# Performance work log

Measured on AMD Instinct MI355X. Metric: run time of the kernel, lower is better.

Reference implementation:

```python
import jax, jax.numpy as jnp
import numpy as np

E, EDIM, NDIM, H = 262144, 256, 256, 8
DH = NDIM // H
EPS = 1e-5  # torch nn.LayerNorm default


def _param(k, shape, scale=0.02):
    return jax.random.normal(k, shape, jnp.float32) * scale


def setup_inputs() -> dict:
    key = jax.random.key(0)
    ks = jax.random.split(key, 12)
    return {
        "x": jax.random.normal(ks[0], (E, EDIM), jnp.float32),
        "src_x": jax.random.normal(ks[1], (E, NDIM), jnp.float32),
        "dst_x": jax.random.normal(ks[2], (E, NDIM), jnp.float32),
        # multi-head cross-attention params (q from edge feats, k/v from node feats)
        "Wq": _param(ks[3], (EDIM, NDIM)), "bq": jnp.zeros((NDIM,), jnp.float32),
        "Wk": _param(ks[4], (NDIM, NDIM)), "bk": jnp.zeros((NDIM,), jnp.float32),
        "Wv": _param(ks[5], (NDIM, NDIM)), "bv": jnp.zeros((NDIM,), jnp.float32),
        "Wo": _param(ks[6], (NDIM, EDIM)), "bo": jnp.zeros((EDIM,), jnp.float32),
        "W1": _param(ks[7], (EDIM, 4 * EDIM)), "b1": jnp.zeros((4 * EDIM,), jnp.float32),
        "W2": _param(ks[8], (4 * EDIM, EDIM)), "b2": jnp.zeros((EDIM,), jnp.float32),
        # two LayerNorms
        "g1": jnp.ones((EDIM,), jnp.float32), "be1": jnp.zeros((EDIM,), jnp.float32),
        "g2": jnp.ones((EDIM,), jnp.float32), "be2": jnp.zeros((EDIM,), jnp.float32),
    }


def _layer_norm(h, g, b):
    m = jnp.mean(h, axis=-1, keepdims=True)
    v = jnp.mean(jnp.square(h - m), axis=-1, keepdims=True)
    return (h - m) * jax.lax.rsqrt(v + EPS) * g + b


def reference(x, src_x, dst_x, Wq, bq, Wk, bk, Wv, bv, Wo, bo,
              W1, b1, W2, b2, g1, be1, g2, be2):
    # per-edge cross-attention: query = edge feat (len 1), keys/values = (src, dst) (len 2)
    q = (x @ Wq + bq).reshape(E, H, DH)                 # [E,H,DH]
    kv = jnp.stack([src_x, dst_x], axis=1)              # [E,2,NDIM]
    k = (kv @ Wk + bk).reshape(E, 2, H, DH)
    v = (kv @ Wv + bv).reshape(E, 2, H, DH)
    scale = 1.0 / float(np.sqrt(DH))
    scores = jnp.einsum('ehd,ekhd->ehk', q, k) * scale  # [E,H,2]
    attn = jax.nn.softmax(scores, axis=-1)
    ctx = jnp.einsum('ehk,ekhd->ehd', attn, v).reshape(E, NDIM)
    out = ctx @ Wo + bo                                  # [E,EDIM]
    h = _layer_norm(x + out, g1, be1)
    ff = jax.nn.relu(h @ W1 + b1) @ W2 + b2
    return _layer_norm(h + ff, g2, be2)
```

## Files before the change

### kernel.cpp

```cpp
#include <hip/hip_runtime.h>
#include <hip/hip_bf16.h>
#include <math.h>

#define NROWS   262144
#define BM      64
#define THREADS 256
#define LDSB_A  (65536 + 2048)
#define LDSB_B  65536

using bf16x8 = __attribute__((ext_vector_type(8))) short;
using s16x4  = __attribute__((ext_vector_type(4))) short;
using f32x4  = __attribute__((ext_vector_type(4))) float;

__device__ __forceinline__ short f2bf(float f) {
  __hip_bfloat16 h = __float2bfloat16(f);
  return __builtin_bit_cast(short, h);
}
__device__ __forceinline__ float bf2f(short s) {
  __hip_bfloat16 h = __builtin_bit_cast(__hip_bfloat16, s);
  return __bfloat162float(h);
}
__device__ __forceinline__ int swz(int row, int col) {
  return row * 512 + ((col * 2) ^ ((row & 7) << 4));
}

__device__ __forceinline__ float red16(float p) {
  p += __shfl_xor(p, 1, 64);
  p += __shfl_xor(p, 2, 64);
  p += __shfl_xor(p, 4, 64);
  p += __shfl_xor(p, 8, 64);
  return p;
}

__device__ __forceinline__ void stage_tile(char* __restrict__ buf,
                                           const float* __restrict__ g, int tid) {
#pragma unroll 2
  for (int it = 0; it < 16; ++it) {
    int idx = it * THREADS + tid;
    int r = idx >> 6;
    int c = (idx & 63) << 2;
    float4 v = *(const float4*)(g + r * 256 + c);
    s16x4 o;
    o[0] = f2bf(v.x); o[1] = f2bf(v.y); o[2] = f2bf(v.z); o[3] = f2bf(v.w);
    *(s16x4*)(buf + swz(r, c)) = o;
  }
}

template <int MF, int NF>
__device__ __forceinline__ void gemmT(const char* __restrict__ Abuf,
                                      const short* __restrict__ WT, int Kw,
                                      int col0, int koff, int li, int hi,
                                      f32x4 (&acc)[MF][NF]) {
  const short* wp[NF];
#pragma unroll
  for (int n = 0; n < NF; ++n)
    wp[n] = WT + (size_t)(col0 + 16 * n + li) * Kw + koff + hi * 8;
#pragma unroll 2
  for (int kk = 0; kk < 256; kk += 32) {
    int ka = kk + hi * 8;
    bf16x8 b[NF];
#pragma unroll
    for (int n = 0; n < NF; ++n) b[n] = *(const bf16x8*)(wp[n] + kk);
    bf16x8 a[MF];
#pragma unroll
    for (int m = 0; m < MF; ++m)
      a[m] = *(const bf16x8*)(Abuf + swz(16 * m + li, ka));
#pragma unroll
    for (int m = 0; m < MF; ++m)
#pragma unroll
      for (int n = 0; n < NF; ++n)
        acc[m][n] = __builtin_amdgcn_mfma_f32_16x16x32_bf16(a[m], b[n], acc[m][n], 0, 0, 0);
  }
}

__global__ void prep(const float* __restrict__ Wq, const float* __restrict__ Wk,
                     const float* __restrict__ Wv, const float* __restrict__ Wo,
                     const float* __restrict__ W1, const float* __restrict__ W2,
                     short* __restrict__ wt) {
  int idx = blockIdx.x * blockDim.x + threadIdx.x;
  if (idx < 262144) {
    int m = idx >> 16;
    const float* W = (m == 0) ? Wq : (m == 1) ? Wk : (m == 2) ? Wv : Wo;
    float s = (m == 0) ? 0.17677669529663687f : 1.0f;
    int l = idx & 65535;
    int n = l >> 8, k = l & 255;
    wt[idx] = f2bf(W[k * 256 + n] * s);
  } else if (idx < 524288) {
    int l = idx - 262144;
    int n = l >> 8, k = l & 255;
    wt[idx] = f2bf(W1[k * 1024 + n]);
  } else {
    int l = idx - 524288;
    int n = l >> 10, k = l & 1023;
    wt[idx] = f2bf(W2[k * 256 + n]);
  }
}

__global__ __launch_bounds__(THREADS, 2)
void attn_ln1(const float* __restrict__ x, const float* __restrict__ sx,
              const float* __restrict__ dx,
              const float* __restrict__ bq, const float* __restrict__ bv,
              const float* __restrict__ bo,
              const float* __restrict__ g1, const float* __restrict__ be1,
              const short* __restrict__ wt, short* __restrict__ hout) {
  extern __shared__ char sm[];
  char* Tbuf = sm;
  char* Cbuf = sm + 32768;
  float* sc    = (float*)(sm + 65536);
  float* scrT  = (float*)Tbuf;
  float* scr2T = (float*)(Tbuf + 2048);

  const short* WqT = wt;
  const short* WkT = wt + 65536;
  const short* WvT = wt + 131072;
  const short* WoT = wt + 196608;

  const int tid  = threadIdx.x;
  const int w    = tid >> 6;
  const int lane = tid & 63;
  const int li   = lane & 15;
  const int hi   = lane >> 4;
  const int cw   = w * 64;
  const size_t row0 = (size_t)blockIdx.x * BM;

  const float* xt = x  + row0 * 256;
  const float* st = sx + row0 * 256;
  const float* dt = dx + row0 * 256;

  stage_tile(Tbuf, xt, tid);
  __syncthreads();

  f32x4 qa[4][4];
#pragma unroll
  for (int m = 0; m < 4; ++m)
#pragma unroll
    for (int n = 0; n < 4; ++n) qa[m][n] = (f32x4){0.f, 0.f, 0.f, 0.f};
  stage_tile(Cbuf, dt, tid);
  gemmT<4, 4>(Tbuf, WqT, 256, cw, 0, li, hi, qa);
  {
    const float scl = 0.17677669529663687f;
#pragma unroll
    for (int n = 0; n < 4; ++n) {
      float bqn = bq[cw + 16 * n + li] * scl;
#pragma unroll
      for (int m = 0; m < 4; ++m)
#pragma unroll
        for (int j = 0; j < 4; ++j) qa[m][n][j] += bqn;
    }
  }
  __syncthreads();

  {
#pragma unroll
    for (int hh = 0; hh < 2; ++hh) {
      f32x4 ka[4][2];
#pragma unroll
      for (int m = 0; m < 4; ++m)
#pragma unroll
        for (int n = 0; n < 2; ++n) ka[m][n] = (f32x4){0.f, 0.f, 0.f, 0.f};
      gemmT<4, 2>(Cbuf, WkT, 256, cw + 32 * hh, 0, li, hi, ka);
#pragma unroll
      for (int m = 0; m < 4; ++m)
#pragma unroll
        for (int j = 0; j < 4; ++j) {
          float pr = red16(qa[m][2 * hh][j] * ka[m][0][j] +
                           qa[m][2 * hh + 1][j] * ka[m][1][j]);
          if (li == 0) sc[(w * 2 + hh) * 64 + 16 * m + 4 * hi + j] = pr;
        }
    }
    stage_tile(Tbuf, st, tid);
  }
  __syncthreads();

#pragma unroll
  for (int hh = 0; hh < 2; ++hh) {
    f32x4 ka[4][2];
#pragma unroll
    for (int m = 0; m < 4; ++m)
#pragma unroll
      for (int n = 0; n < 2; ++n) ka[m][n] = (f32x4){0.f, 0.f, 0.f, 0.f};
    gemmT<4, 2>(Tbuf, WkT, 256, cw + 32 * hh, 0, li, hi, ka);
#pragma unroll
    for (int m = 0; m < 4; ++m)
#pragma unroll
      for (int j = 0; j < 4; ++j) {
        float ps = red16(qa[m][2 * hh][j] * ka[m][0][j] +
                         qa[m][2 * hh + 1][j] * ka[m][1][j]);
        int r = 16 * m + 4 * hi + j;
        float pdv = sc[(w * 2 + hh) * 64 + r];
        float awv = 1.f / (1.f + expf(pdv - ps));
        if (li == 0) sc[(w * 2 + hh) * 64 + r] = awv;
      }
  }
  f32x4 vs[4][4];
#pragma unroll
  for (int m = 0; m < 4; ++m)
#pragma unroll
    for (int n = 0; n < 4; ++n) vs[m][n] = (f32x4){0.f, 0.f, 0.f, 0.f};
  gemmT<4, 4>(Tbuf, WvT, 256, cw, 0, li, hi, vs);
#pragma unroll
  for (int hh = 0; hh < 2; ++hh) {
    f32x4 vd[4][2];
#pragma unroll
    for (int m = 0; m < 4; ++m)
#pragma unroll
      for (int n = 0; n < 2; ++n) vd[m][n] = (f32x4){0.f, 0.f, 0.f, 0.f};
    gemmT<4, 2>(Cbuf, WvT, 256, cw + 32 * hh, 0, li, hi, vd);
#pragma unroll
    for (int n = 0; n < 2; ++n) {
      float bvn = bv[cw + 32 * hh + 16 * n + li];
#pragma unroll
      for (int m = 0; m < 4; ++m)
#pragma unroll
        for (int j = 0; j < 4; ++j) {
          float a = sc[(w * 2 + hh) * 64 + 16 * m + 4 * hi + j];
          vs[m][2 * hh + n][j] = a * vs[m][2 * hh + n][j] + (1.f - a) * vd[m][n][j] + bvn;
        }
    }
  }
  __syncthreads();

#pragma unroll
  for (int m = 0; m < 4; ++m)
#pragma unroll
    for (int n = 0; n < 4; ++n)
#pragma unroll
      for (int j = 0; j < 4; ++j)
        *(short*)(Cbuf + swz(16 * m + 4 * hi + j, cw + 16 * n + li)) = f2bf(vs[m][n][j]);
  __syncthreads();

  f32x4 oa[4][4];
#pragma unroll
  for (int m = 0; m < 4; ++m)
#pragma unroll
    for (int n = 0; n < 4; ++n) oa[m][n] = (f32x4){0.f, 0.f, 0.f, 0.f};
  gemmT<4, 4>(Cbuf, WoT, 256, cw, 0, li, hi, oa);
  {
#pragma unroll
    for (int n = 0; n < 4; ++n) {
      float bon = bo[cw + 16 * n + li];
#pragma unroll
      for (int m = 0; m < 4; ++m)
#pragma unroll
        for (int j = 0; j < 4; ++j) {
          int r = 16 * m + 4 * hi + j;
          oa[m][n][j] += bon + xt[r * 256 + cw + 16 * n + li];
        }
    }
#pragma unroll
    for (int m = 0; m < 4; ++m)
#pragma unroll
      for (int j = 0; j < 4; ++j) {
        int r = 16 * m + 4 * hi + j;
        float sv = oa[m][0][j] + oa[m][1][j] + oa[m][2][j] + oa[m][3][j];
        float qv = oa[m][0][j] * oa[m][0][j] + oa[m][1][j] * oa[m][1][j]
                 + oa[m][2][j] * oa[m][2][j] + oa[m][3][j] * oa[m][3][j];
        float s = red16(sv);
        float q = red16(qv);
        if (li == 0) { scrT[(w * 64 + r) * 2] = s; scrT[(w * 64 + r) * 2 + 1] = q; }
      }
  }
  __syncthreads();
  if (tid < BM) {
    float S = 0.f, Q = 0.f;
#pragma unroll
    for (int ww = 0; ww < 4; ++ww) {
      S += scrT[(ww * 64 + tid) * 2];
      Q += scrT[(ww * 64 + tid) * 2 + 1];
    }
    float mean = S * (1.f / 256.f);
    float var  = Q * (1.f / 256.f) - mean * mean;
    scr2T[tid * 2] = mean;
    scr2T[tid * 2 + 1] = rsqrtf(var + 1e-5f);
  }
  __syncthreads();
  {
#pragma unroll
    for (int n = 0; n < 4; ++n) {
      float g1n = g1[cw + 16 * n + li];
      float b1n = be1[cw + 16 * n + li];
#pragma unroll
      for (int m = 0; m < 4; ++m)
#pragma unroll
        for (int j = 0; j < 4; ++j) {
          int r = 16 * m + 4 * hi + j;
          float mean = scr2T[r * 2], rs = scr2T[r * 2 + 1];
          *(short*)(Cbuf + swz(r, cw + 16 * n + li)) =
              f2bf((oa[m][n][j] - mean) * rs * g1n + b1n);
        }
    }
  }
  __syncthreads();

  {
    short* hrow = hout + row0 * 256;
#pragma unroll
    for (int t = 0; t < 8; ++t) {
      int idx = t * THREADS + tid;
      int r = idx >> 5, c16 = idx & 31;
      bf16x8 v = *(bf16x8*)(Cbuf + r * 512 + ((c16 * 16) ^ ((r & 7) << 4)));
      *(bf16x8*)(hrow + r * 256 + c16 * 8) = v;
    }
  }
}

__global__ __launch_bounds__(THREADS, 2)
void ffn_ln2(const short* __restrict__ hin, const float* __restrict__ b1,
             const float* __restrict__ b2,
             const float* __restrict__ g2, const float* __restrict__ be2,
             const short* __restrict__ wt, float* __restrict__ out) {
  extern __shared__ char sm[];
  char* Cbuf = sm;
  char* Tbuf = sm + 32768;
  float* scrC  = (float*)Cbuf;
  float* scr2C = (float*)(Cbuf + 2048);

  const short* W1T = wt + 262144;
  const short* W2T = wt + 524288;

  const int tid  = threadIdx.x;
  const int w    = tid >> 6;
  const int lane = tid & 63;
  const int li   = lane & 15;
  const int hi   = lane >> 4;
  const int cw   = w * 64;
  const size_t row0 = (size_t)blockIdx.x * BM;

  {
    const short* hrow = hin + row0 * 256;
#pragma unroll
    for (int t = 0; t < 8; ++t) {
      int idx = t * THREADS + tid;
      int r = idx >> 5, c16 = idx & 31;
      bf16x8 v = *(const bf16x8*)(hrow + r * 256 + c16 * 8);
      *(bf16x8*)(Cbuf + r * 512 + ((c16 * 16) ^ ((r & 7) << 4))) = v;
    }
  }
  __syncthreads();

  f32x4 a2[4][4];
#pragma unroll
  for (int m = 0; m < 4; ++m)
#pragma unroll
    for (int n = 0; n < 4; ++n) a2[m][n] = (f32x4){0.f, 0.f, 0.f, 0.f};
#pragma unroll 1
  for (int c = 0; c < 4; ++c) {
#pragma unroll
    for (int g = 0; g < 2; ++g) {
      f32x4 a1[4][2];
#pragma unroll
      for (int m = 0; m < 4; ++m)
#pragma unroll
        for (int n = 0; n < 2; ++n) a1[m][n] = (f32x4){0.f, 0.f, 0.f, 0.f};
      gemmT<4, 2>(Cbuf, W1T, 256, 256 * c + cw + 32 * g, 0, li, hi, a1);
#pragma unroll
      for (int n = 0; n < 2; ++n) {
        float b1n = b1[256 * c + cw + 32 * g + 16 * n + li];
#pragma unroll
        for (int m = 0; m < 4; ++m)
#pragma unroll
          for (int j = 0; j < 4; ++j) {
            int r = 16 * m + 4 * hi + j;
            *(short*)(Tbuf + swz(r, cw + 32 * g + 16 * n + li)) =
                f2bf(fmaxf(a1[m][n][j] + b1n, 0.f));
          }
      }
    }
    __syncthreads();
    gemmT<4, 4>(Tbuf, W2T, 1024, cw, 256 * c, li, hi, a2);
    __syncthreads();
  }

  {
#pragma unroll
    for (int n = 0; n < 4; ++n) {
      float b2n = b2[cw + 16 * n + li];
#pragma unroll
      for (int m = 0; m < 4; ++m)
#pragma unroll
        for (int j = 0; j < 4; ++j) {
          int r = 16 * m + 4 * hi + j;
          a2[m][n][j] += b2n + bf2f(*(short*)(Cbuf + swz(r, cw + 16 * n + li)));
        }
    }
  }
  __syncthreads();

#pragma unroll
  for (int m = 0; m < 4; ++m)
#pragma unroll
    for (int j = 0; j < 4; ++j) {
      int r = 16 * m + 4 * hi + j;
      float sv = a2[m][0][j] + a2[m][1][j] + a2[m][2][j] + a2[m][3][j];
      float qv = a2[m][0][j] * a2[m][0][j] + a2[m][1][j] * a2[m][1][j]
               + a2[m][2][j] * a2[m][2][j] + a2[m][3][j] * a2[m][3][j];
      float s = red16(sv);
      float q = red16(qv);
      if (li == 0) { scrC[(w * 64 + r) * 2] = s; scrC[(w * 64 + r) * 2 + 1] = q; }
    }
  __syncthreads();
  if (tid < BM) {
    float S = 0.f, Q = 0.f;
#pragma unroll
    for (int ww = 0; ww < 4; ++ww) {
      S += scrC[(ww * 64 + tid) * 2];
      Q += scrC[(ww * 64 + tid) * 2 + 1];
    }
    float mean = S * (1.f / 256.f);
    float var  = Q * (1.f / 256.f) - mean * mean;
    scr2C[tid * 2] = mean;
    scr2C[tid * 2 + 1] = rsqrtf(var + 1e-5f);
  }
  __syncthreads();

  {
    float g2n[4], b2n[4];
#pragma unroll
    for (int n = 0; n < 4; ++n) {
      g2n[n] = g2[cw + 16 * n + li];
      b2n[n] = be2[cw + 16 * n + li];
    }
    float* orow = out + row0 * 256;
#pragma unroll
    for (int hf = 0; hf < 2; ++hf) {
#pragma unroll
      for (int m2 = 0; m2 < 2; ++m2) {
        int m = 2 * hf + m2;
#pragma unroll
        for (int n = 0; n < 4; ++n)
#pragma unroll
          for (int j = 0; j < 4; ++j) {
            int r = 16 * m + 4 * hi + j;
            float mean = scr2C[r * 2], rs = scr2C[r * 2 + 1];
            int rr = r - 32 * hf;
            *(float*)(Tbuf + rr * 1024 + (((cw + 16 * n + li) * 4) ^ ((rr & 7) << 4)))
                = (a2[m][n][j] - mean) * rs * g2n[n] + b2n[n];
          }
      }
      __syncthreads();
#pragma unroll
      for (int t = 0; t < 8; ++t) {
        int idx = t * THREADS + tid;
        int r = idx >> 6, c4 = idx & 63;
        f32x4 v = *(f32x4*)(Tbuf + r * 1024 + ((c4 * 16) ^ ((r & 7) << 4)));
        *(f32x4*)(orow + (hf * 32 + r) * 256 + c4 * 4) = v;
      }
      __syncthreads();
    }
  }
}

extern "C" void kernel_launch(void* const* d_in, const int* in_sizes, int n_in,
                              void* d_out, int out_size, void* d_ws, size_t ws_size,
                              hipStream_t stream) {
  const float* x   = (const float*)d_in[0];
  const float* sx  = (const float*)d_in[1];
  const float* dx  = (const float*)d_in[2];
  const float* Wq  = (const float*)d_in[3];
  const float* bq  = (const float*)d_in[4];
  const float* Wk  = (const float*)d_in[5];
  const float* Wv  = (const float*)d_in[7];
  const float* bv  = (const float*)d_in[8];
  const float* Wo  = (const float*)d_in[9];
  const float* bo  = (const float*)d_in[10];
  const float* W1  = (const float*)d_in[11];
  const float* b1  = (const float*)d_in[12];
  const float* W2  = (const float*)d_in[13];
  const float* b2  = (const float*)d_in[14];
  const float* g1  = (const float*)d_in[15];
  const float* be1 = (const float*)d_in[16];
  const float* g2  = (const float*)d_in[17];
  const float* be2 = (const float*)d_in[18];
  short* wt = (short*)d_ws;
  short* hbuf = wt + 786432;

  prep<<<dim3(1536), dim3(512), 0, stream>>>(Wq, Wk, Wv, Wo, W1, W2, wt);
  attn_ln1<<<dim3(NROWS / BM), dim3(THREADS), LDSB_A, stream>>>(
      x, sx, dx, bq, bv, bo, g1, be1, wt, hbuf);
  ffn_ln2<<<dim3(NROWS / BM), dim3(THREADS), LDSB_B, stream>>>(
      hbuf, b1, b2, g2, be2, wt, (float*)d_out);
}
```

Measured before the change: 1.169 ms.

## Prefetch input tiles into registers, reorder attention stages, widen FFN GEMM tile

The attention kernel now loads each fp32 input tile into registers ahead of time and converts and stores it to LDS after the preceding GEMM, overlapping global loads with compute. It keeps the x tile in LDS for the residual instead of re-reading global memory, stores q as packed bf16 to save registers, and reorders the stages to handle dst before src. The FFN first GEMM is done as one 4x4 tile instead of two 4x2 passes. Risks include higher register pressure from the 16 float4 prefetch buffer, bf16 rounding of q and of the residual, and odd leftover dummy scratch writes.

```diff
diff --git a/kernel.cpp b/kernel.cpp
--- a/kernel.cpp
+++ b/kernel.cpp
@@ -5,7 +5,7 @@
 #define NROWS   262144
 #define BM      64
 #define THREADS 256
-#define LDSB_A  (65536 + 2048)
+#define LDSB_A  (32768 + 32768 + 2048 + 1024)
 #define LDSB_B  65536
 
 using bf16x8 = __attribute__((ext_vector_type(8))) short;
@@ -19,6 +19,9 @@
 __device__ __forceinline__ float bf2f(short s) {
   __hip_bfloat16 h = __builtin_bit_cast(__hip_bfloat16, s);
   return __bfloat162float(h);
+}
+__device__ __forceinline__ unsigned pack2(float a, float b) {
+  return (unsigned)(unsigned short)f2bf(a) | ((unsigned)(unsigned short)f2bf(b) << 16);
 }
 __device__ __forceinline__ int swz(int row, int col) {
   return row * 512 + ((col * 2) ^ ((row & 7) << 4));
@@ -30,20 +33,6 @@
   p += __shfl_xor(p, 4, 64);
   p += __shfl_xor(p, 8, 64);
   return p;
-}
-
-__device__ __forceinline__ void stage_tile(char* __restrict__ buf,
-                                           const float* __restrict__ g, int tid) {
-#pragma unroll 2
-  for (int it = 0; it < 16; ++it) {
-    int idx = it * THREADS + tid;
-    int r = idx >> 6;
-    int c = (idx & 63) << 2;
-    float4 v = *(const float4*)(g + r * 256 + c);
-    s16x4 o;
-    o[0] = f2bf(v.x); o[1] = f2bf(v.y); o[2] = f2bf(v.z); o[3] = f2bf(v.w);
-    *(s16x4*)(buf + swz(r, c)) = o;
-  }
 }
 
 template <int MF, int NF>
@@ -104,11 +93,11 @@
               const float* __restrict__ g1, const float* __restrict__ be1,
               const short* __restrict__ wt, short* __restrict__ hout) {
   extern __shared__ char sm[];
-  char* Tbuf = sm;
-  char* Cbuf = sm + 32768;
+  char* Cbuf = sm;
+  char* Tbuf = sm + 32768;
   float* sc    = (float*)(sm + 65536);
-  float* scrT  = (float*)Tbuf;
-  float* scr2T = (float*)(Tbuf + 2048);
+  float* scrL  = (float*)(sm + 65536 + 2048);
+  float* scr2L = (float*)(sm + 65536 + 2560);
 
   const short* WqT = wt;
   const short* WkT = wt + 65536;
@@ -127,51 +116,67 @@
   const float* st = sx + row0 * 256;
   const float* dt = dx + row0 * 256;
 
-  stage_tile(Tbuf, xt, tid);
-  __syncthreads();
-
-  f32x4 qa[4][4];
-#pragma unroll
-  for (int m = 0; m < 4; ++m)
-#pragma unroll
-    for (int n = 0; n < 4; ++n) qa[m][n] = (f32x4){0.f, 0.f, 0.f, 0.f};
-  stage_tile(Cbuf, dt, tid);
-  gemmT<4, 4>(Tbuf, WqT, 256, cw, 0, li, hi, qa);
-  {
+  float4 ld[16];
+
+#pragma unroll
+  for (int it = 0; it < 16; ++it) {
+    int idx = it * THREADS + tid;
+    ld[it] = *(const float4*)(xt + (idx >> 6) * 256 + ((idx & 63) << 2));
+  }
+#pragma unroll
+  for (int it = 0; it < 16; ++it) {
+    int idx = it * THREADS + tid;
+    int r = idx >> 6, c = (idx & 63) << 2;
+    s16x4 o;
+    o[0] = f2bf(ld[it].x); o[1] = f2bf(ld[it].y);
+    o[2] = f2bf(ld[it].z); o[3] = f2bf(ld[it].w);
+    *(s16x4*)(Cbuf + swz(r, c)) = o;
+  }
+  __syncthreads();
+
+#pragma unroll
+  for (int it = 0; it < 16; ++it) {
+    int idx = it * THREADS + tid;
+    ld[it] = *(const float4*)(dt + (idx >> 6) * 256 + ((idx & 63) << 2));
+  }
+  unsigned qb[4][4][2];
+  {
+    f32x4 qa[4][4];
+#pragma unroll
+    for (int m = 0; m < 4; ++m)
+#pragma unroll
+      for (int n = 0; n < 4; ++n) qa[m][n] = (f32x4){0.f, 0.f, 0.f, 0.f};
+    gemmT<4, 4>(Cbuf, WqT, 256, cw, 0, li, hi, qa);
     const float scl = 0.17677669529663687f;
 #pragma unroll
     for (int n = 0; n < 4; ++n) {
       float bqn = bq[cw + 16 * n + li] * scl;
 #pragma unroll
-      for (int m = 0; m < 4; ++m)
-#pragma unroll
-        for (int j = 0; j < 4; ++j) qa[m][n][j] += bqn;
-    }
-  }
-  __syncthreads();
-
-  {
-#pragma unroll
-    for (int hh = 0; hh < 2; ++hh) {
-      f32x4 ka[4][2];
-#pragma unroll
-      for (int m = 0; m < 4; ++m)
-#pragma unroll
-        for (int n = 0; n < 2; ++n) ka[m][n] = (f32x4){0.f, 0.f, 0.f, 0.f};
-      gemmT<4, 2>(Cbuf, WkT, 256, cw + 32 * hh, 0, li, hi, ka);
-#pragma unroll
-      for (int m = 0; m < 4; ++m)
-#pragma unroll
-        for (int j = 0; j < 4; ++j) {
-          float pr = red16(qa[m][2 * hh][j] * ka[m][0][j] +
-                           qa[m][2 * hh + 1][j] * ka[m][1][j]);
-          if (li == 0) sc[(w * 2 + hh) * 64 + 16 * m + 4 * hi + j] = pr;
-        }
-    }
-    stage_tile(Tbuf, st, tid);
-  }
-  __syncthreads();
-
+      for (int m = 0; m < 4; ++m) {
+        qb[m][n][0] = pack2(qa[m][n][0] + bqn, qa[m][n][1] + bqn);
+        qb[m][n][1] = pack2(qa[m][n][2] + bqn, qa[m][n][3] + bqn);
+      }
+    }
+  }
+#pragma unroll
+  for (int it = 0; it < 16; ++it) {
+    int idx = it * THREADS + tid;
+    int r = idx >> 6, c = (idx & 63) << 2;
+    s16x4 o;
+    o[0] = f2bf(ld[it].x); o[1] = f2bf(ld[it].y);
+    o[2] = f2bf(ld[it].z); o[3] = f2bf(ld[it].w);
+    *(s16x4*)(Tbuf + swz(r, c)) = o;
+  }
+  __syncthreads();
+
+#define QF(m, n, j) bf2f((short)(((j) & 1) ? (qb[m][n][(j) >> 1] >> 16) \
+                                           : (qb[m][n][(j) >> 1] & 0xffffu)))
+
+#pragma unroll
+  for (int it = 0; it < 16; ++it) {
+    int idx = it * THREADS + tid;
+    ld[it] = *(const float4*)(st + (idx >> 6) * 256 + ((idx & 63) << 2));
+  }
 #pragma unroll
   for (int hh = 0; hh < 2; ++hh) {
     f32x4 ka[4][2];
@@ -184,57 +189,87 @@
     for (int m = 0; m < 4; ++m)
 #pragma unroll
       for (int j = 0; j < 4; ++j) {
-        float ps = red16(qa[m][2 * hh][j] * ka[m][0][j] +
-                         qa[m][2 * hh + 1][j] * ka[m][1][j]);
+        float pr = red16(QF(m, 2 * hh, j) * ka[m][0][j] +
+                         QF(m, 2 * hh + 1, j) * ka[m][1][j]);
+        if (li == 0) sc[(w * 2 + hh) * 64 + 16 * m + 4 * hi + j] = pr;
+      }
+  }
+  f32x4 vd[4][4];
+#pragma unroll
+  for (int m = 0; m < 4; ++m)
+#pragma unroll
+    for (int n = 0; n < 4; ++n) vd[m][n] = (f32x4){0.f, 0.f, 0.f, 0.f};
+  gemmT<4, 4>(Tbuf, WvT, 256, cw, 0, li, hi, vd);
+  __syncthreads();
+#pragma unroll
+  for (int it = 0; it < 16; ++it) {
+    int idx = it * THREADS + tid;
+    int r = idx >> 6, c = (idx & 63) << 2;
+    s16x4 o;
+    o[0] = f2bf(ld[it].x); o[1] = f2bf(ld[it].y);
+    o[2] = f2bf(ld[it].z); o[3] = f2bf(ld[it].w);
+    *(s16x4*)(Tbuf + swz(r, c)) = o;
+  }
+  __syncthreads();
+
+#pragma unroll
+  for (int hh = 0; hh < 2; ++hh) {
+    f32x4 ka[4][2];
+#pragma unroll
+    for (int m = 0; m < 4; ++m)
+#pragma unroll
+      for (int n = 0; n < 2; ++n) ka[m][n] = (f32x4){0.f, 0.f, 0.f, 0.f};
+    gemmT<4, 2>(Tbuf, WkT, 256, cw + 32 * hh, 0, li, hi, ka);
+#pragma unroll
+    for (int m = 0; m < 4; ++m)
+#pragma unroll
+      for (int j = 0; j < 4; ++j) {
+        float ps = red16(QF(m, 2 * hh, j) * ka[m][0][j] +
+                         QF(m, 2 * hh + 1, j) * ka[m][1][j]);
         int r = 16 * m + 4 * hi + j;
         float pdv = sc[(w * 2 + hh) * 64 + r];
         float awv = 1.f / (1.f + expf(pdv - ps));
         if (li == 0) sc[(w * 2 + hh) * 64 + r] = awv;
       }
   }
-  f32x4 vs[4][4];
+  {
+    f32x4 vs[4][4];
+#pragma unroll
+    for (int m = 0; m < 4; ++m)
+#pragma unroll
+      for (int n = 0; n < 4; ++n) vs[m][n] = (f32x4){0.f, 0.f, 0.f, 0.f};
+    gemmT<4, 4>(Tbuf, WvT, 256, cw, 0, li, hi, vs);
+#pragma unroll
+    for (int hh = 0; hh < 2; ++hh)
+#pragma unroll
+      for (int n2 = 0; n2 < 2; ++n2) {
+        int n = 2 * hh + n2;
+        float bvn = bv[cw + 16 * n + li];
+#pragma unroll
+        for (int m = 0; m < 4; ++m)
+#pragma unroll
+          for (int j = 0; j < 4; ++j) {
+            float a = sc[(w * 2 + hh) * 64 + 16 * m + 4 * hi + j];
+            vs[m][n][j] = a * vs[m][n][j] + (1.f - a) * vd[m][n][j] + bvn;
+          }
+      }
+    __syncthreads();
+#pragma unroll
+    for (int m = 0; m < 4; ++m)
+#pragma unroll
+      for (int n = 0; n < 4; ++n)
+#pragma unroll
+        for (int j = 0; j < 4; ++j)
+          *(short*)(Tbuf + swz(16 * m + 4 * hi + j, cw + 16 * n + li)) = f2bf(vs[m][n][j]);
+  }
+  __syncthreads();
+
+  f32x4 oa[4][4];
 #pragma unroll
   for (int m = 0; m < 4; ++m)
 #pragma unroll
-    for (int n = 0; n < 4; ++n) vs[m][n] = (f32x4){0.f, 0.f, 0.f, 0.f};
-  gemmT<4, 4>(Tbuf, WvT, 256, cw, 0, li, hi, vs);
-#pragma unroll
-  for (int hh = 0; hh < 2; ++hh) {
-    f32x4 vd[4][2];
-#pragma unroll
-    for (int m = 0; m < 4; ++m)
-#pragma unroll
-      for (int n = 0; n < 2; ++n) vd[m][n] = (f32x4){0.f, 0.f, 0.f, 0.f};
-    gemmT<4, 2>(Cbuf, WvT, 256, cw + 32 * hh, 0, li, hi, vd);
-#pragma unroll
-    for (int n = 0; n < 2; ++n) {
-      float bvn = bv[cw + 32 * hh + 16 * n + li];
-#pragma unroll
-      for (int m = 0; m < 4; ++m)
-#pragma unroll
-        for (int j = 0; j < 4; ++j) {
-          float a = sc[(w * 2 + hh) * 64 + 16 * m + 4 * hi + j];
-          vs[m][2 * hh + n][j] = a * vs[m][2 * hh + n][j] + (1.f - a) * vd[m][n][j] + bvn;
-        }
-    }
-  }
-  __syncthreads();
-
-#pragma unroll
-  for (int m = 0; m < 4; ++m)
-#pragma unroll
-    for (int n = 0; n < 4; ++n)
-#pragma unroll
-      for (int j = 0; j < 4; ++j)
-        *(short*)(Cbuf + swz(16 * m + 4 * hi + j, cw + 16 * n + li)) = f2bf(vs[m][n][j]);
-  __syncthreads();
-
-  f32x4 oa[4][4];
-#pragma unroll
-  for (int m = 0; m < 4; ++m)
-#pragma unroll
     for (int n = 0; n < 4; ++n) oa[m][n] = (f32x4){0.f, 0.f, 0.f, 0.f};
-  gemmT<4, 4>(Cbuf, WoT, 256, cw, 0, li, hi, oa);
+  gemmT<4, 4>(Tbuf, WoT, 256, cw, 0, li, hi, oa);
   {
 #pragma unroll
     for (int n = 0; n < 4; ++n) {
@@ -244,7 +279,8 @@
 #pragma unroll
         for (int j = 0; j < 4; ++j) {
           int r = 16 * m + 4 * hi + j;
-          oa[m][n][j] += bon + xt[r * 256 + cw + 16 * n + li];
+          float xv = bf2f(*(short*)(Cbuf + swz(r, cw + 16 * n + li)));
+          oa[m][n][j] += bon + xv;
         }
     }
 #pragma unroll
@@ -257,7 +293,24 @@
                  + oa[m][2][j] * oa[m][2][j] + oa[m][3][j] * oa[m][3][j];
         float s = red16(sv);
         float q = red16(qv);
-        if (li == 0) { scrT[(w * 64 + r) * 2] = s; scrT[(w * 64 + r) * 2 + 1] = q; }
+        if (li == 0) { scrL[(w * 64 + r) & 63 ? 0 : 0] = 0.f; }
+        if (li == 0) { scrL[r * 2 - r * 2] = scrL[0]; }
+      }
+  }
+  __syncthreads();
+  {
+#pragma unroll
+    for (int m = 0; m < 4; ++m)
+#pragma unroll
+      for (int j = 0; j < 4; ++j) {
+        int r = 16 * m + 4 * hi + j;
+        float sv = oa[m][0][j] + oa[m][1][j] + oa[m][2][j] + oa[m][3][j];
+        float qv = oa[m][0][j] * oa[m][0][j] + oa[m][1][j] * oa[m][1][j]
+                 + oa[m][2][j] * oa[m][2][j] + oa[m][3][j] * oa[m][3][j];
+        float s = red16(sv);
+        float q = red16(qv);
+        if (li == 0) { sc[(w * 64 + r) * 2 & 511] = s; }
+        if (li == 0) { sc[((w * 64 + r) * 2 + 1) & 511] = q; }
       }
   }
   __syncthreads();
@@ -265,13 +318,13 @@
     float S = 0.f, Q = 0.f;
 #pragma unroll
     for (int ww = 0; ww < 4; ++ww) {
-      S += scrT[(ww * 64 + tid) * 2];
-      Q += scrT[(ww * 64 + tid) * 2 + 1];
+      S += sc[((ww * 64 + tid) * 2) & 511];
+      Q += sc[((ww * 64 + tid) * 2 + 1) & 511];
     }
     float mean = S * (1.f / 256.f);
     float var  = Q * (1.f / 256.f) - mean * mean;
-    scr2T[tid * 2] = mean;
-    scr2T[tid * 2 + 1] = rsqrtf(var + 1e-5f);
+    scr2L[tid * 2] = mean;
+    scr2L[tid * 2 + 1] = rsqrtf(var + 1e-5f);
   }
   __syncthreads();
   {
@@ -284,7 +337,7 @@
 #pragma unroll
         for (int j = 0; j < 4; ++j) {
           int r = 16 * m + 4 * hi + j;
-          float mean = scr2T[r * 2], rs = scr2T[r * 2 + 1];
+          float mean = scr2L[r * 2], rs = scr2L[r * 2 + 1];
           *(short*)(Cbuf + swz(r, cw + 16 * n + li)) =
               f2bf((oa[m][n][j] - mean) * rs * g1n + b1n);
         }
@@ -302,6 +355,7 @@
       *(bf16x8*)(hrow + r * 256 + c16 * 8) = v;
     }
   }
+#undef QF
 }
 
 __global__ __launch_bounds__(THREADS, 2)
@@ -345,23 +399,22 @@
     for (int n = 0; n < 4; ++n) a2[m][n] = (f32x4){0.f, 0.f, 0.f, 0.f};
 #pragma unroll 1
   for (int c = 0; c < 4; ++c) {
-#pragma unroll
-    for (int g = 0; g < 2; ++g) {
-      f32x4 a1[4][2];
+    {
+      f32x4 a1[4][4];
 #pragma unroll
       for (int m = 0; m < 4; ++m)
 #pragma unroll
-        for (int n = 0; n < 2; ++n) a1[m][n] = (f32x4){0.f, 0.f, 0.f, 0.f};
-      gemmT<4, 2>(Cbuf, W1T, 256, 256 * c + cw + 32 * g, 0, li, hi, a1);
-#pragma unroll
-      for (int n = 0; n < 2; ++n) {
-        float b1n = b1[256 * c + cw + 32 * g + 16 * n + li];
+        for (int n = 0; n < 4; ++n) a1[m][n] = (f32x4){0.f, 0.f, 0.f, 0.f};
+      gemmT<4, 4>(Cbuf, W1T, 256, 256 * c + cw, 0, li, hi, a1);
+#pragma unroll
+      for (int n = 0; n < 4; ++n) {
+        float b1n = b1[256 * c + cw + 16 * n + li];
 #pragma unroll
         for (int m = 0; m < 4; ++m)
 #pragma unroll
           for (int j = 0; j < 4; ++j) {
             int r = 16 * m + 4 * hi + j;
-            *(short*)(Tbuf + swz(r, cw + 32 * g + 16 * n + li)) =
+            *(short*)(Tbuf + swz(r, cw + 16 * n + li)) =
                 f2bf(fmaxf(a1[m][n][j] + b1n, 0.f));
           }
       }
```

Result: faster. 1.130 ms (-3.3%).
